# Kernel tuning notes

Measured on AMD Instinct MI355X. Metric: run time of the kernel, lower is better.

## Reference

```python
import jax, jax.numpy as jnp
import numpy as np


def setup_inputs() -> dict:
    key = jax.random.key(0)
    k1, k2, k3 = jax.random.split(key, 3)
    B, T, S, D = 16, 1024, 1024, 1024
    inp = jax.random.normal(k1, (B, T, D), dtype=jnp.float32)
    ctx = jax.random.normal(k2, (B, S, D), dtype=jnp.float32)
    # nn.Linear(dim, dim, bias=False) weight, applied as x @ W.T
    W_in = jax.random.normal(k3, (D, D), dtype=jnp.float32) * (1.0 / np.sqrt(D))
    return {"input": inp, "context": ctx, "W_in": W_in}


def reference(input, context, W_in):
    # h_t = linear_in(input): [B,T,D] @ W_in.T
    h_t = jnp.einsum("btd,ed->bte", input, W_in)
    # align scores: [B,T,S]
    align = jnp.einsum("btd,bsd->bts", h_t, context)
    align_vectors = jax.nn.softmax(align, axis=-1)
    # context-weighted sum: [B,T,D]
    attn_h = jnp.einsum("bts,bsd->btd", align_vectors, context)
    # non-one-step path: transpose(0,1)
    attn_h = jnp.transpose(attn_h, (1, 0, 2))          # [T,B,D]
    align_vectors = jnp.transpose(align_vectors, (1, 0, 2))  # [T,B,S]
    return attn_h, align_vectors
```

## Files before the change

### kernel.cpp

```cpp
#include <hip/hip_runtime.h>
#include <hip/hip_bf16.h>

using short8 = __attribute__((ext_vector_type(8))) short;
using half8  = __attribute__((ext_vector_type(8))) _Float16;
using f32x4  = __attribute__((ext_vector_type(4))) float;

constexpr int Bdim = 16;
constexpr int Tdim = 1024;
constexpr int Sdim = 1024;
constexpr int Ddim = 1024;

__device__ __forceinline__ unsigned short f2hu(float x) {
  _Float16 h = (_Float16)x;
  return __builtin_bit_cast(unsigned short, h);
}
__device__ __forceinline__ float hu2f(unsigned short u) {
  return (float)__builtin_bit_cast(_Float16, u);
}

__global__ void __launch_bounds__(256)
conv_kernel(const float* __restrict__ src, unsigned short* __restrict__ dst, int n4) {
  int i = blockIdx.x * blockDim.x + threadIdx.x;
  int stride = gridDim.x * blockDim.x;
  for (; i < n4; i += stride) {
    float4 v = reinterpret_cast<const float4*>(src)[i];
    ushort4 h;
    h.x = f2hu(v.x); h.y = f2hu(v.y); h.z = f2hu(v.z); h.w = f2hu(v.w);
    reinterpret_cast<ushort4*>(dst)[i] = h;
  }
}

__global__ void __launch_bounds__(256)
ctxprep_kernel(const float* __restrict__ ctx, unsigned short* __restrict__ ctx16,
               unsigned short* __restrict__ ctxT) {
  __shared__ float tile[64][65];
  int b = blockIdx.z;
  int d0 = blockIdx.x * 64, s0 = blockIdx.y * 64;
  const float* src = ctx + (size_t)b * Sdim * Ddim;
  unsigned short* dstS = ctx16 + (size_t)b * Sdim * Ddim;
  unsigned short* dstT = ctxT + (size_t)b * Ddim * Sdim;
  int tx = threadIdx.x & 15, ty = threadIdx.x >> 4;
  #pragma unroll
  for (int r = 0; r < 4; ++r) {
    int s = ty + r * 16;
    float4 v = reinterpret_cast<const float4*>(src + (size_t)(s0 + s) * Ddim + d0)[tx];
    ushort4 hs;
    hs.x = f2hu(v.x); hs.y = f2hu(v.y); hs.z = f2hu(v.z); hs.w = f2hu(v.w);
    reinterpret_cast<ushort4*>(dstS + (size_t)(s0 + s) * Ddim + d0)[tx] = hs;
    tile[s][tx * 4 + 0] = v.x; tile[s][tx * 4 + 1] = v.y;
    tile[s][tx * 4 + 2] = v.z; tile[s][tx * 4 + 3] = v.w;
  }
  __syncthreads();
  #pragma unroll
  for (int r = 0; r < 4; ++r) {
    int d = ty + r * 16;
    ushort4 o;
    o.x = f2hu(tile[tx * 4 + 0][d]);
    o.y = f2hu(tile[tx * 4 + 1][d]);
    o.z = f2hu(tile[tx * 4 + 2][d]);
    o.w = f2hu(tile[tx * 4 + 3][d]);
    reinterpret_cast<ushort4*>(dstT + (size_t)(d0 + d) * Sdim + s0)[tx] = o;
  }
}

#define MFMAH(d, x, y)                                                          \
  d = __builtin_amdgcn_mfma_f32_16x16x32_f16(__builtin_bit_cast(half8, (x)),    \
                                             __builtin_bit_cast(half8, (y)), (d), 0, 0, 0)

#define GLOADLDS(g, l)                                                          \
  __builtin_amdgcn_global_load_lds((const __attribute__((address_space(1))) void*)(g), \
                                   (__attribute__((address_space(3))) void*)(l), 16, 0, 0)

template <int MODE>
__global__ void __launch_bounds__(512, 2)
gemmP(const unsigned short* __restrict__ Ag, const unsigned short* __restrict__ Bg,
      size_t aBatch, size_t bBatch, int mnShift,
      unsigned short* __restrict__ outH, float* __restrict__ outF) {
  constexpr int NT = 16;
  __shared__ __align__(16) unsigned short lds[2 * 2 * 16384];

  const int hw = blockIdx.x;
  const int L  = (hw & 7) * 32 + (hw >> 3);
  const int bb = L >> mnShift;
  const int r  = L & ((1 << mnShift) - 1);
  const int m0 = (r >> 2) * 256;
  const int n0 = (r & 3) * 256;

  const int tid  = threadIdx.x;
  const int lane = tid & 63;
  const int w    = tid >> 6;
  const int wr   = (w >> 2) * 128;
  const int wc   = (w & 3) * 64;
  const int l15  = lane & 15;
  const int g0   = lane >> 4;
  const int r7   = l15 & 7;

  const int srow8 = tid >> 3;
  const int sg    = tid & 7;
  const int rs    = srow8 & 7;
  const unsigned short* spA = Ag + (size_t)bb * aBatch + (size_t)(m0 + srow8) * 1024 + ((sg ^ rs) * 8);
  const unsigned short* spB = Bg + (size_t)bb * bBatch + (size_t)(n0 + srow8) * 1024 + ((sg ^ rs) * 8);

  auto stage = [&](int buf, int kt) {
    #pragma unroll
    for (int i = 0; i < 4; ++i) {
      unsigned short* lb = lds + buf * 32768 + (srow8 + i * 64) * 64 + sg * 8;
      GLOADLDS(spA + (size_t)i * (64 * 1024) + kt * 64, lb);
      GLOADLDS(spB + (size_t)i * (64 * 1024) + kt * 64, lb + 16384);
    }
  };

  f32x4 acc[8][4];
  const f32x4 vzero = {0.f, 0.f, 0.f, 0.f};
  #pragma unroll
  for (int f = 0; f < 8; ++f)
    #pragma unroll
    for (int j = 0; j < 4; ++j) acc[f][j] = vzero;

  stage(0, 0);
  stage(1, 1);
  asm volatile("s_waitcnt vmcnt(8)" ::: "memory");
  __builtin_amdgcn_s_barrier();

  #pragma unroll 1
  for (int t = 0; t < NT; ++t) {
    const unsigned short* tb = lds + (t & 1) * 32768;
    const unsigned short* tB = tb + 16384;

    short8 bf[4][2], af[8][2];
    #pragma unroll
    for (int j = 0; j < 4; ++j)
      #pragma unroll
      for (int kk = 0; kk < 2; ++kk) {
        const int row = wc + j * 16 + l15;
        bf[j][kk] = *reinterpret_cast<const short8*>(tB + row * 64 + ((kk * 4 + g0) ^ r7) * 8);
      }
    #pragma unroll
    for (int f = 0; f < 8; ++f)
      #pragma unroll
      for (int kk = 0; kk < 2; ++kk) {
        const int row = wr + f * 16 + l15;
        af[f][kk] = *reinterpret_cast<const short8*>(tb + row * 64 + ((kk * 4 + g0) ^ r7) * 8);
      }
    asm volatile("s_waitcnt lgkmcnt(0)" ::: "memory");
    __builtin_amdgcn_sched_barrier(0);
    __builtin_amdgcn_s_barrier();

    if (t + 2 < NT) stage(t & 1, t + 2);

    __builtin_amdgcn_s_setprio(1);
    #pragma unroll
    for (int f = 0; f < 8; ++f)
      #pragma unroll
      for (int j = 0; j < 4; ++j)
        #pragma unroll
        for (int kk = 0; kk < 2; ++kk)
          MFMAH(acc[f][j], af[f][kk], bf[j][kk]);
    __builtin_amdgcn_s_setprio(0);
    __builtin_amdgcn_sched_barrier(0);

    if (t + 2 < NT) asm volatile("s_waitcnt vmcnt(8)" ::: "memory");
    else            asm volatile("s_waitcnt vmcnt(0)" ::: "memory");
    __builtin_amdgcn_s_barrier();
  }

  const int lr = (lane >> 4) * 4;
  const int lc = lane & 15;
  #pragma unroll
  for (int f = 0; f < 8; ++f)
    #pragma unroll
    for (int j = 0; j < 4; ++j)
      #pragma unroll
      for (int q = 0; q < 4; ++q) {
        int rr = m0 + wr + f * 16 + lr + q;
        int cc = n0 + wc + j * 16 + lc;
        float v = acc[f][j][q];
        if constexpr (MODE == 2) {
          outH[(size_t)rr * 1024 + cc] = f2hu(v);
        } else {
          outF[((size_t)rr * 16 + bb) * 1024 + cc] = v;
        }
      }
}

__global__ void __launch_bounds__(512, 2)
gemmF(const unsigned short* __restrict__ Hh, const unsigned short* __restrict__ Cg,
      float* __restrict__ alignOut, unsigned short* __restrict__ pOut) {
  constexpr int NT = 16;
  __shared__ __align__(16) unsigned short lds[2 * 4096 + 65536];

  const int hw = blockIdx.x;
  const int L  = (hw & 7) * 32 + (hw >> 3);
  const int bb = L >> 4;
  const int m0 = (L & 15) * 64;

  const int tid  = threadIdx.x;
  const int lane = tid & 63;
  const int w    = tid >> 6;
  const int l15  = lane & 15;
  const int g0   = lane >> 4;

  const int srow = tid >> 3;
  const int sg   = tid & 7;
  const int rs   = srow & 7;
  const unsigned short* spA = Hh + (size_t)bb * (Tdim * Ddim) + (size_t)(m0 + srow) * 1024 + ((sg ^ rs) * 8);
  const unsigned short* spB = Cg + (size_t)bb * (Sdim * Ddim) + (size_t)srow * 1024 + ((sg ^ rs) * 8);

  unsigned short* const ldsB = lds + 8192;

  auto stageA = [&](int buf, int kt) {
    GLOADLDS(spA + kt * 64, lds + buf * 4096 + tid * 8);
  };
  auto stageB = [&](int kt) {
    #pragma unroll
    for (int i = 0; i < 16; ++i)
      GLOADLDS(spB + (size_t)i * (64 * 1024) + kt * 64, ldsB + i * 4096 + tid * 8);
  };

  f32x4 acc[4][8];
  const f32x4 vzero = {0.f, 0.f, 0.f, 0.f};
  #pragma unroll
  for (int f = 0; f < 4; ++f)
    #pragma unroll
    for (int j = 0; j < 8; ++j) acc[f][j] = vzero;

  stageA(0, 0);
  stageB(0);
  stageA(1, 1);
  asm volatile("s_waitcnt vmcnt(1)" ::: "memory");
  __builtin_amdgcn_s_barrier();

  #pragma unroll 1
  for (int t = 0; t < NT; ++t) {
    const unsigned short* tA = lds + (t & 1) * 4096;

    short8 bf[8][2];
    #pragma unroll
    for (int j = 0; j < 8; ++j) {
      const int row = w * 128 + j * 16 + l15;
      #pragma unroll
      for (int kk = 0; kk < 2; ++kk)
        bf[j][kk] = *reinterpret_cast<const short8*>(ldsB + row * 64 + ((kk * 4 + g0) ^ (row & 7)) * 8);
    }
    short8 af[4][2];
    #pragma unroll
    for (int f = 0; f < 4; ++f) {
      const int row = f * 16 + l15;
      #pragma unroll
      for (int kk = 0; kk < 2; ++kk)
        af[f][kk] = *reinterpret_cast<const short8*>(tA + row * 64 + ((kk * 4 + g0) ^ (row & 7)) * 8);
    }
    asm volatile("s_waitcnt lgkmcnt(0)" ::: "memory");
    __builtin_amdgcn_sched_barrier(0);
    __builtin_amdgcn_s_barrier();

    if (t + 1 < NT) stageB(t + 1);
    if (t + 2 < NT) stageA(t & 1, t + 2);

    __builtin_amdgcn_s_setprio(1);
    #pragma unroll
    for (int f = 0; f < 4; ++f)
      #pragma unroll
      for (int j = 0; j < 8; ++j)
        #pragma unroll
        for (int kk = 0; kk < 2; ++kk)
          MFMAH(acc[f][j], af[f][kk], bf[j][kk]);
    __builtin_amdgcn_s_setprio(0);

    if (t + 1 < NT) {
      if (t + 2 < NT) asm volatile("s_waitcnt vmcnt(1)" ::: "memory");
      else            asm volatile("s_waitcnt vmcnt(0)" ::: "memory");
    }
    __builtin_amdgcn_s_barrier();
  }

  float* red = (float*)lds;
  const int lr = (lane >> 4) * 4;

  float rmax[4][4];
  #pragma unroll
  for (int f = 0; f < 4; ++f)
    #pragma unroll
    for (int q = 0; q < 4; ++q) {
      float m = acc[f][0][q];
      #pragma unroll
      for (int j = 1; j < 8; ++j) m = fmaxf(m, acc[f][j][q]);
      #pragma unroll
      for (int o = 1; o < 16; o <<= 1) m = fmaxf(m, __shfl_xor(m, o));
      rmax[f][q] = m;
    }
  if (l15 == 0) {
    #pragma unroll
    for (int f = 0; f < 4; ++f)
      #pragma unroll
      for (int q = 0; q < 4; ++q) red[(f * 16 + lr + q) * 8 + w] = rmax[f][q];
  }
  __syncthreads();
  #pragma unroll
  for (int f = 0; f < 4; ++f)
    #pragma unroll
    for (int q = 0; q < 4; ++q) {
      const float* rr = red + (f * 16 + lr + q) * 8;
      float m = rr[0];
      #pragma unroll
      for (int k = 1; k < 8; ++k) m = fmaxf(m, rr[k]);
      rmax[f][q] = m;
    }
  __syncthreads();

  float rsum[4][4];
  #pragma unroll
  for (int f = 0; f < 4; ++f)
    #pragma unroll
    for (int q = 0; q < 4; ++q) {
      float s = 0.f;
      #pragma unroll
      for (int j = 0; j < 8; ++j) {
        float e = __expf(acc[f][j][q] - rmax[f][q]);
        acc[f][j][q] = e;
        s += e;
      }
      #pragma unroll
      for (int o = 1; o < 16; o <<= 1) s += __shfl_xor(s, o);
      rsum[f][q] = s;
    }
  if (l15 == 0) {
    #pragma unroll
    for (int f = 0; f < 4; ++f)
      #pragma unroll
      for (int q = 0; q < 4; ++q) red[(f * 16 + lr + q) * 8 + w] = rsum[f][q];
  }
  __syncthreads();
  #pragma unroll
  for (int f = 0; f < 4; ++f)
    #pragma unroll
    for (int q = 0; q < 4; ++q) {
      const float* rr = red + (f * 16 + lr + q) * 8;
      float s = ((rr[0] + rr[1]) + (rr[2] + rr[3])) + ((rr[4] + rr[5]) + (rr[6] + rr[7]));
      rsum[f][q] = 1.0f / s;
    }

  #pragma unroll
  for (int f = 0; f < 4; ++f)
    #pragma unroll
    for (int q = 0; q < 4; ++q) {
      const int row = m0 + f * 16 + lr + q;
      float inv = rsum[f][q];
      #pragma unroll
      for (int j = 0; j < 8; ++j) {
        const int cc = w * 128 + j * 16 + l15;
        float v = acc[f][j][q] * inv;
        alignOut[((size_t)row * 16 + bb) * 1024 + cc] = v;
        pOut[((size_t)bb * 1024 + row) * 1024 + cc] = f2hu(v);
      }
    }
}

extern "C" void kernel_launch(void* const* d_in, const int* in_sizes, int n_in,
                              void* d_out, int out_size, void* d_ws, size_t ws_size,
                              hipStream_t stream) {
  const float* input = (const float*)d_in[0];
  const float* ctx   = (const float*)d_in[1];
  const float* Wt    = (const float*)d_in[2];
  float* attn_out  = (float*)d_out;
  float* align_out = attn_out + (size_t)Tdim * Bdim * Ddim;

  const size_t NE = (size_t)Bdim * Tdim * Ddim;
  unsigned short* x16  = (unsigned short*)d_ws;
  unsigned short* Wh   = x16 + NE;
  unsigned short* hh   = Wh + (size_t)Ddim * Ddim;
  unsigned short* ctxT = hh + NE;
  unsigned short* ctx16 = x16;
  unsigned short* p     = hh;

  conv_kernel<<<2048, 256, 0, stream>>>(input, x16, (int)(NE / 4));
  conv_kernel<<<512, 256, 0, stream>>>(Wt, Wh, (int)((size_t)Ddim * Ddim / 4));
  gemmP<2><<<256, 512, 0, stream>>>(x16, Wh, 0, 0, 8, hh, nullptr);
  ctxprep_kernel<<<dim3(16, 16, Bdim), 256, 0, stream>>>(ctx, ctx16, ctxT);
  gemmF<<<256, 512, 0, stream>>>(hh, ctx16, align_out, p);
  gemmP<1><<<256, 512, 0, stream>>>(p, ctxT, (size_t)Tdim * Sdim,
                                    (size_t)Ddim * Sdim, 4, nullptr, attn_out);
}
```

Measured before the change: 186.9 us.

## Switch GEMM to single-buffered 128-wide K tiles with split-phase loads

Replaces the double-buffered 64-wide K pipeline (16 iterations) with a single LDS buffer holding 128-wide K tiles (8 iterations). Each iteration reads the first half of the K tile and runs MFMAs, reads the second half, then issues the next tile's global-to-LDS loads while the second MFMA batch runs. This halves the number of barriers and loop iterations and widens the XOR swizzle to 16 groups. The cost is less prefetch depth: it waits on vmcnt(0) at the top of every iteration, so load latency is only hidden behind one half of the MFMA work.

```diff
diff --git a/kernel.cpp b/kernel.cpp
--- a/kernel.cpp
+++ b/kernel.cpp
@@ -76,8 +76,8 @@
 gemmP(const unsigned short* __restrict__ Ag, const unsigned short* __restrict__ Bg,
       size_t aBatch, size_t bBatch, int mnShift,
       unsigned short* __restrict__ outH, float* __restrict__ outF) {
-  constexpr int NT = 16;
-  __shared__ __align__(16) unsigned short lds[2 * 2 * 16384];
+  constexpr int NT = 8;
+  __shared__ __align__(16) unsigned short lds[65536];
 
   const int hw = blockIdx.x;
   const int L  = (hw & 7) * 32 + (hw >> 3);
@@ -93,20 +93,20 @@
   const int wc   = (w & 3) * 64;
   const int l15  = lane & 15;
   const int g0   = lane >> 4;
-  const int r7   = l15 & 7;
-
-  const int srow8 = tid >> 3;
-  const int sg    = tid & 7;
-  const int rs    = srow8 & 7;
-  const unsigned short* spA = Ag + (size_t)bb * aBatch + (size_t)(m0 + srow8) * 1024 + ((sg ^ rs) * 8);
-  const unsigned short* spB = Bg + (size_t)bb * bBatch + (size_t)(n0 + srow8) * 1024 + ((sg ^ rs) * 8);
-
-  auto stage = [&](int buf, int kt) {
-    #pragma unroll
-    for (int i = 0; i < 4; ++i) {
-      unsigned short* lb = lds + buf * 32768 + (srow8 + i * 64) * 64 + sg * 8;
-      GLOADLDS(spA + (size_t)i * (64 * 1024) + kt * 64, lb);
-      GLOADLDS(spB + (size_t)i * (64 * 1024) + kt * 64, lb + 16384);
+
+  const int srow16 = tid >> 4;
+  const int sg     = tid & 15;
+  const int rs     = srow16 & 15;
+  const unsigned short* spA = Ag + (size_t)bb * aBatch + (size_t)(m0 + srow16) * 1024 + ((sg ^ rs) * 8);
+  const unsigned short* spB = Bg + (size_t)bb * bBatch + (size_t)(n0 + srow16) * 1024 + ((sg ^ rs) * 8);
+  unsigned short* const ldA = lds + srow16 * 128 + sg * 8;
+  unsigned short* const ldB = ldA + 32768;
+
+  auto stage = [&](int kt) {
+    #pragma unroll
+    for (int i = 0; i < 8; ++i) {
+      GLOADLDS(spA + (size_t)i * (32 * 1024) + kt * 128, ldA + i * 4096);
+      GLOADLDS(spB + (size_t)i * (32 * 1024) + kt * 128, ldB + i * 4096);
     }
   };
 
@@ -117,37 +117,32 @@
     #pragma unroll
     for (int j = 0; j < 4; ++j) acc[f][j] = vzero;
 
-  stage(0, 0);
-  stage(1, 1);
-  asm volatile("s_waitcnt vmcnt(8)" ::: "memory");
-  __builtin_amdgcn_s_barrier();
+  stage(0);
 
   #pragma unroll 1
   for (int t = 0; t < NT; ++t) {
-    const unsigned short* tb = lds + (t & 1) * 32768;
-    const unsigned short* tB = tb + 16384;
-
-    short8 bf[4][2], af[8][2];
-    #pragma unroll
-    for (int j = 0; j < 4; ++j)
-      #pragma unroll
-      for (int kk = 0; kk < 2; ++kk) {
-        const int row = wc + j * 16 + l15;
-        bf[j][kk] = *reinterpret_cast<const short8*>(tB + row * 64 + ((kk * 4 + g0) ^ r7) * 8);
-      }
-    #pragma unroll
-    for (int f = 0; f < 8; ++f)
-      #pragma unroll
-      for (int kk = 0; kk < 2; ++kk) {
-        const int row = wr + f * 16 + l15;
-        af[f][kk] = *reinterpret_cast<const short8*>(tb + row * 64 + ((kk * 4 + g0) ^ r7) * 8);
-      }
+    asm volatile("s_waitcnt vmcnt(0)" ::: "memory");
+    __builtin_amdgcn_s_barrier();
+    asm volatile("" ::: "memory");
+
+    short8 af[8][2], bf[4][2];
+
+    #pragma unroll
+    for (int j = 0; j < 4; ++j) {
+      const int row = wc + j * 16 + l15;
+      #pragma unroll
+      for (int kk = 0; kk < 2; ++kk)
+        bf[j][kk] = *reinterpret_cast<const short8*>(lds + 32768 + row * 128 + ((kk * 4 + g0) ^ l15) * 8);
+    }
+    #pragma unroll
+    for (int f = 0; f < 8; ++f) {
+      const int row = wr + f * 16 + l15;
+      #pragma unroll
+      for (int kk = 0; kk < 2; ++kk)
+        af[f][kk] = *reinterpret_cast<const short8*>(lds + row * 128 + ((kk * 4 + g0) ^ l15) * 8);
+    }
     asm volatile("s_waitcnt lgkmcnt(0)" ::: "memory");
     __builtin_amdgcn_sched_barrier(0);
-    __builtin_amdgcn_s_barrier();
-
-    if (t + 2 < NT) stage(t & 1, t + 2);
-
     __builtin_amdgcn_s_setprio(1);
     #pragma unroll
     for (int f = 0; f < 8; ++f)
@@ -159,9 +154,35 @@
     __builtin_amdgcn_s_setprio(0);
     __builtin_amdgcn_sched_barrier(0);
 
-    if (t + 2 < NT) asm volatile("s_waitcnt vmcnt(8)" ::: "memory");
-    else            asm volatile("s_waitcnt vmcnt(0)" ::: "memory");
+    #pragma unroll
+    for (int j = 0; j < 4; ++j) {
+      const int row = wc + j * 16 + l15;
+      #pragma unroll
+      for (int kk = 0; kk < 2; ++kk)
+        bf[j][kk] = *reinterpret_cast<const short8*>(lds + 32768 + row * 128 + (((kk + 2) * 4 + g0) ^ l15) * 8);
+    }
+    #pragma unroll
+    for (int f = 0; f < 8; ++f) {
+      const int row = wr + f * 16 + l15;
+      #pragma unroll
+      for (int kk = 0; kk < 2; ++kk)
+        af[f][kk] = *reinterpret_cast<const short8*>(lds + row * 128 + (((kk + 2) * 4 + g0) ^ l15) * 8);
+    }
+    asm volatile("s_waitcnt lgkmcnt(0)" ::: "memory");
+    __builtin_amdgcn_sched_barrier(0);
     __builtin_amdgcn_s_barrier();
+
+    if (t + 1 < NT) stage(t + 1);
+
+    __builtin_amdgcn_s_setprio(1);
+    #pragma unroll
+    for (int f = 0; f < 8; ++f)
+      #pragma unroll
+      for (int j = 0; j < 4; ++j)
+        #pragma unroll
+        for (int kk = 0; kk < 2; ++kk)
+          MFMAH(acc[f][j], af[f][kk], bf[j][kk]);
+    __builtin_amdgcn_s_setprio(0);
   }
 
   const int lr = (lane >> 4) * 4;
```

After: 183.0 us, median of 2. -2.1%, faster.

## Shrink GEMM tiles to 128x128 and launch four times more blocks

Applied to the files above, without the earlier changes.

Replaces the 256x256-tile GEMM with a 128x128-tile version that runs 1024 blocks instead of 256 and allows 4 blocks per CU. LDS use per block drops by half. The pipeline changes from staging two tiles ahead with one barrier per step to staging one tile ahead with a barrier before each compute step. The aim is to fill all CUs better, since 256 large blocks underfill the 256-CU device, at the cost of lower data reuse per block and more global traffic.

```diff
diff --git a/kernel.cpp b/kernel.cpp
--- a/kernel.cpp
+++ b/kernel.cpp
@@ -72,104 +72,103 @@
                                    (__attribute__((address_space(3))) void*)(l), 16, 0, 0)
 
 template <int MODE>
-__global__ void __launch_bounds__(512, 2)
-gemmP(const unsigned short* __restrict__ Ag, const unsigned short* __restrict__ Bg,
+__global__ void __launch_bounds__(512, 4)
+gemmQ(const unsigned short* __restrict__ Ag, const unsigned short* __restrict__ Bg,
       size_t aBatch, size_t bBatch, int mnShift,
       unsigned short* __restrict__ outH, float* __restrict__ outF) {
   constexpr int NT = 16;
-  __shared__ __align__(16) unsigned short lds[2 * 2 * 16384];
+  __shared__ __align__(16) unsigned short lds[2 * 16384];
 
   const int hw = blockIdx.x;
-  const int L  = (hw & 7) * 32 + (hw >> 3);
+  const int L  = (hw & 7) * 128 + (hw >> 3);
   const int bb = L >> mnShift;
   const int r  = L & ((1 << mnShift) - 1);
-  const int m0 = (r >> 2) * 256;
-  const int n0 = (r & 3) * 256;
+  const int m0 = (r >> 3) * 128;
+  const int n0 = (r & 7) * 128;
 
   const int tid  = threadIdx.x;
   const int lane = tid & 63;
   const int w    = tid >> 6;
-  const int wr   = (w >> 2) * 128;
-  const int wc   = (w & 3) * 64;
+  const int wr   = (w >> 2) * 64;
+  const int wc   = (w & 3) * 32;
   const int l15  = lane & 15;
   const int g0   = lane >> 4;
   const int r7   = l15 & 7;
 
-  const int srow8 = tid >> 3;
-  const int sg    = tid & 7;
-  const int rs    = srow8 & 7;
-  const unsigned short* spA = Ag + (size_t)bb * aBatch + (size_t)(m0 + srow8) * 1024 + ((sg ^ rs) * 8);
-  const unsigned short* spB = Bg + (size_t)bb * bBatch + (size_t)(n0 + srow8) * 1024 + ((sg ^ rs) * 8);
+  const int crow = lane >> 3;
+  const int cg   = (lane & 7) ^ crow;
+  const int ca   = w * 2;
+  const unsigned short* pA0 = Ag + (size_t)bb * aBatch + (size_t)(m0 + ca * 8 + crow) * 1024 + cg * 8;
+  const unsigned short* pA1 = pA0 + 8 * 1024;
+  const unsigned short* pB0 = Bg + (size_t)bb * bBatch + (size_t)(n0 + ca * 8 + crow) * 1024 + cg * 8;
+  const unsigned short* pB1 = pB0 + 8 * 1024;
+  const int d0 = ca * 512 + lane * 8;
+  const int d1 = d0 + 512;
 
   auto stage = [&](int buf, int kt) {
-    #pragma unroll
-    for (int i = 0; i < 4; ++i) {
-      unsigned short* lb = lds + buf * 32768 + (srow8 + i * 64) * 64 + sg * 8;
-      GLOADLDS(spA + (size_t)i * (64 * 1024) + kt * 64, lb);
-      GLOADLDS(spB + (size_t)i * (64 * 1024) + kt * 64, lb + 16384);
-    }
+    unsigned short* base = lds + buf * 16384;
+    GLOADLDS(pA0 + kt * 64, base + d0);
+    GLOADLDS(pA1 + kt * 64, base + d1);
+    GLOADLDS(pB0 + kt * 64, base + 8192 + d0);
+    GLOADLDS(pB1 + kt * 64, base + 8192 + d1);
   };
 
-  f32x4 acc[8][4];
+  f32x4 acc[4][2];
   const f32x4 vzero = {0.f, 0.f, 0.f, 0.f};
   #pragma unroll
-  for (int f = 0; f < 8; ++f)
-    #pragma unroll
-    for (int j = 0; j < 4; ++j) acc[f][j] = vzero;
+  for (int f = 0; f < 4; ++f) { acc[f][0] = vzero; acc[f][1] = vzero; }
 
   stage(0, 0);
-  stage(1, 1);
-  asm volatile("s_waitcnt vmcnt(8)" ::: "memory");
-  __builtin_amdgcn_s_barrier();
 
   #pragma unroll 1
   for (int t = 0; t < NT; ++t) {
-    const unsigned short* tb = lds + (t & 1) * 32768;
-    const unsigned short* tB = tb + 16384;
-
-    short8 bf[4][2], af[8][2];
-    #pragma unroll
-    for (int j = 0; j < 4; ++j)
-      #pragma unroll
-      for (int kk = 0; kk < 2; ++kk) {
-        const int row = wc + j * 16 + l15;
+    if (t + 1 < NT) {
+      stage((t + 1) & 1, t + 1);
+      asm volatile("s_waitcnt vmcnt(4)" ::: "memory");
+    } else {
+      asm volatile("s_waitcnt vmcnt(0)" ::: "memory");
+    }
+    __builtin_amdgcn_s_barrier();
+    asm volatile("" ::: "memory");
+    const unsigned short* tb = lds + (t & 1) * 16384;
+    const unsigned short* tB = tb + 8192;
+
+    short8 bf[2][2], af[4][2];
+    #pragma unroll
+    for (int j = 0; j < 2; ++j) {
+      const int row = wc + j * 16 + l15;
+      #pragma unroll
+      for (int kk = 0; kk < 2; ++kk)
         bf[j][kk] = *reinterpret_cast<const short8*>(tB + row * 64 + ((kk * 4 + g0) ^ r7) * 8);
-      }
-    #pragma unroll
-    for (int f = 0; f < 8; ++f)
-      #pragma unroll
-      for (int kk = 0; kk < 2; ++kk) {
-        const int row = wr + f * 16 + l15;
+    }
+    #pragma unroll
+    for (int f = 0; f < 4; ++f) {
+      const int row = wr + f * 16 + l15;
+      #pragma unroll
+      for (int kk = 0; kk < 2; ++kk)
         af[f][kk] = *reinterpret_cast<const short8*>(tb + row * 64 + ((kk * 4 + g0) ^ r7) * 8);
-      }
+    }
     asm volatile("s_waitcnt lgkmcnt(0)" ::: "memory");
     __builtin_amdgcn_sched_barrier(0);
-    __builtin_amdgcn_s_barrier();
-
-    if (t + 2 < NT) stage(t & 1, t + 2);
-
     __builtin_amdgcn_s_setprio(1);
     #pragma unroll
-    for (int f = 0; f < 8; ++f)
-      #pragma unroll
-      for (int j = 0; j < 4; ++j)
+    for (int f = 0; f < 4; ++f)
+      #pragma unroll
+      for (int j = 0; j < 2; ++j)
         #pragma unroll
         for (int kk = 0; kk < 2; ++kk)
           MFMAH(acc[f][j], af[f][kk], bf[j][kk]);
     __builtin_amdgcn_s_setprio(0);
     __builtin_amdgcn_sched_barrier(0);
-
-    if (t + 2 < NT) asm volatile("s_waitcnt vmcnt(8)" ::: "memory");
-    else            asm volatile("s_waitcnt vmcnt(0)" ::: "memory");
     __builtin_amdgcn_s_barrier();
   }
 
   const int lr = (lane >> 4) * 4;
   const int lc = lane & 15;
   #pragma unroll
-  for (int f = 0; f < 8; ++f)
-    #pragma unroll
-    for (int j = 0; j < 4; ++j)
+  for (int f = 0; f < 4; ++f)
+    #pragma unroll
+    for (int j = 0; j < 2; ++j)
       #pragma unroll
       for (int q = 0; q < 4; ++q) {
         int rr = m0 + wr + f * 16 + lr + q;
@@ -375,9 +374,9 @@
 
   conv_kernel<<<2048, 256, 0, stream>>>(input, x16, (int)(NE / 4));
   conv_kernel<<<512, 256, 0, stream>>>(Wt, Wh, (int)((size_t)Ddim * Ddim / 4));
-  gemmP<2><<<256, 512, 0, stream>>>(x16, Wh, 0, 0, 8, hh, nullptr);
+  gemmQ<2><<<1024, 512, 0, stream>>>(x16, Wh, 0, 0, 10, hh, nullptr);
   ctxprep_kernel<<<dim3(16, 16, Bdim), 256, 0, stream>>>(ctx, ctx16, ctxT);
   gemmF<<<256, 512, 0, stream>>>(hh, ctx16, align_out, p);
-  gemmP<1><<<256, 512, 0, stream>>>(p, ctxT, (size_t)Tdim * Sdim,
-                                    (size_t)Ddim * Sdim, 4, nullptr, attn_out);
-}
+  gemmQ<1><<<1024, 512, 0, stream>>>(p, ctxT, (size_t)Tdim * Sdim,
+                                     (size_t)Ddim * Sdim, 6, nullptr, attn_out);
+}
```

New measurement: 186.2 us. About the same (-0.4%).
